# Kernel tuning notes

Hardware: AMD Instinct MI355X
Metric: run time of the kernel (lower is better)

Reference implementation:

```python
import math
import jax, jax.numpy as jnp
import numpy as np

LN_EPS = 1e-5


def _layernorm(x, g, b):
    m = jnp.mean(x, axis=-1, keepdims=True)
    v = jnp.var(x, axis=-1, keepdims=True)
    return (x - m) / jnp.sqrt(v + LN_EPS) * g + b


def setup_inputs() -> dict:
    key = jax.random.key(0)
    ks = jax.random.split(key, 14)
    B, C, H, W = 8, 96, 224, 224
    dim, hidden = 96, int(96 * 4.0)

    def lin(k, i, o):
        return jax.random.normal(k, (i, o), jnp.float32) * 0.02

    return {
        "x": jax.random.normal(ks[0], (B, C, H, W), jnp.float32),
        "entropy_map": jax.random.uniform(ks[1], (B, 1, H, W), jnp.float32),
        "beta": jnp.float32(1.0),
        "wq": lin(ks[2], dim, dim), "bq": jnp.zeros((dim,), jnp.float32),
        "wk": lin(ks[3], dim, dim), "bk": jnp.zeros((dim,), jnp.float32),
        "wv": lin(ks[4], dim, dim), "bv": jnp.zeros((dim,), jnp.float32),
        "wo": lin(ks[5], dim, dim), "bo": jnp.zeros((dim,), jnp.float32),
        "ln1_g": jnp.ones((dim,), jnp.float32), "ln1_b": jnp.zeros((dim,), jnp.float32),
        "ln2_g": jnp.ones((dim,), jnp.float32), "ln2_b": jnp.zeros((dim,), jnp.float32),
        "w_fc1": lin(ks[6], dim, hidden), "b_fc1": jnp.zeros((hidden,), jnp.float32),
        "w_fc2": lin(ks[7], hidden, dim), "b_fc2": jnp.zeros((dim,), jnp.float32),
    }


def reference(x, entropy_map, beta, wq, bq, wk, bk, wv, bv, wo, bo,
              ln1_g, ln1_b, ln2_g, ln2_b, w_fc1, b_fc1, w_fc2, b_fc2):
    B, C, H, W = x.shape
    ws = 7
    num_heads = 4
    hd = C // num_heads
    nHw, nWw = H // ws, W // ws
    N = ws * ws

    # (B,C,H,W) -> (B,H,W,C), norm1
    xt = jnp.transpose(x, (0, 2, 3, 1))
    xn = _layernorm(xt, ln1_g, ln1_b)

    # window partition -> (B*nW, N, C)
    xw = xn.reshape(B, nHw, ws, nWw, ws, C).transpose(0, 1, 3, 2, 4, 5).reshape(-1, N, C)
    ew = entropy_map.transpose(0, 2, 3, 1).reshape(B, nHw, ws, nWw, ws, 1)
    ew = ew.transpose(0, 1, 3, 2, 4, 5).reshape(-1, N, 1)  # (Bw, N, 1)

    Bw = xw.shape[0]
    q = (jnp.einsum('bnc,cd->bnd', xw, wq) + bq).reshape(Bw, N, num_heads, hd).transpose(0, 2, 1, 3)
    k = (jnp.einsum('bnc,cd->bnd', xw, wk) + bk).reshape(Bw, N, num_heads, hd).transpose(0, 2, 1, 3)
    v = (jnp.einsum('bnc,cd->bnd', xw, wv) + bv).reshape(Bw, N, num_heads, hd).transpose(0, 2, 1, 3)

    scores = jnp.einsum('bhqd,bhkd->bhqk', q, k) / math.sqrt(hd)
    attn = jax.nn.softmax(scores, axis=-1)

    # entropy gating: per-query factor (Bw,1,N,1), then renormalize over keys
    gating = jnp.exp(-beta * ew)[:, None, :, :]
    attn = attn * gating
    attn = attn / (jnp.sum(attn, axis=-1, keepdims=True) + 1e-9)

    out = jnp.einsum('bhqk,bhkd->bhqd', attn, v).transpose(0, 2, 1, 3).reshape(Bw, N, C)
    out = jnp.einsum('bnc,cd->bnd', out, wo) + bo

    # window merge -> (B,H,W,C)
    out = out.reshape(B, nHw, nWw, ws, ws, C).transpose(0, 1, 3, 2, 4, 5).reshape(B, H, W, C)

    x_res = xt + out  # (B,H,W,C)

    # MLP branch
    xn2 = _layernorm(x_res, ln2_g, ln2_b)
    h = jax.nn.gelu(jnp.einsum('bhwc,cd->bhwd', xn2, w_fc1) + b_fc1, approximate=False)
    mlp_out = jnp.einsum('bhwd,dc->bhwc', h, w_fc2) + b_fc2

    x_out = x_res + mlp_out
    return jnp.transpose(x_out, (0, 3, 1, 2))  # (B,C,H,W)
```

## Files before the change

### kernel.cpp

```cpp
#include <hip/hip_runtime.h>
#include <hip/hip_bf16.h>
#include <math.h>

typedef __attribute__((ext_vector_type(8))) short short8;
typedef __attribute__((ext_vector_type(4))) float f32x4;
typedef __attribute__((ext_vector_type(4))) unsigned int uint4v;

struct __align__(8) U2 { unsigned int x, y; };

#define DEVI static __device__ __forceinline__

DEVI unsigned pk1(float f){ unsigned u = __float_as_uint(f); return (u + 0x7fffu + ((u>>16)&1u)) >> 16; }
DEVI unsigned pk2(float a, float b){
  __hip_bfloat162 h = __float22bfloat162_rn(float2{a, b});
  union { __hip_bfloat162 h; unsigned u; } c; c.h = h; return c.u;
}
DEVI float bfu(unsigned hs){ return __uint_as_float((hs & 0xffffu) << 16); }

DEVI short8 lds8(const unsigned short* p){
  union { short8 v; U2 u[2]; } f;
  f.u[0] = *(const U2*)p;
  f.u[1] = *(const U2*)(p + 4);
  return f.v;
}
DEVI short8 mk8(unsigned a, unsigned b, unsigned c, unsigned d){
  union { short8 v; unsigned u[4]; } f; f.u[0]=a; f.u[1]=b; f.u[2]=c; f.u[3]=d; return f.v;
}
DEVI short8 zero8(){ return mk8(0,0,0,0); }
DEVI short8 gfrag(const unsigned short* p){ union { short8 v; uint4v u; } f; f.u = *(const uint4v*)p; return f.v; }
DEVI f32x4 MFMA(short8 a, short8 b, f32x4 c){ return __builtin_amdgcn_mfma_f32_16x16x32_bf16(a, b, c, 0, 0, 0); }
DEVI void st2(unsigned short* p, unsigned lo, unsigned hi){ U2 t; t.x=lo; t.y=hi; *(U2*)p = t; }

DEVI float fastrcp(float x){ float r; asm("v_rcp_f32 %0, %1" : "=v"(r) : "v"(x)); return r; }
DEVI float gelu_f(float v){
  float z2 = fmaf(v*v*v, -0.07135481627f, -1.5957691216f*v);
  return v * fastrcp(1.f + __expf(z2));
}

__global__ __launch_bounds__(256) void prep_kernel(
    const float* __restrict__ wq, const float* __restrict__ wk,
    const float* __restrict__ wv, const float* __restrict__ wo,
    const float* __restrict__ w1, const float* __restrict__ w2,
    unsigned short* __restrict__ wfr)
{
  int i = blockIdx.x * 256 + threadIdx.x;
  if (i >= 110592) return;
  int j = i & 7, lane = (i >> 3) & 63, fr = i >> 9;
  int ln = lane & 15, lg = lane >> 4;
  float v;
  if (fr < 18)      { int s = fr;       int mt = s/3,  kb = s%3;  v = wq[(32*kb + 8*lg + j)*96  + 16*mt + ln] * 0.20412414523193150818f; }
  else if (fr < 36) { int s = fr - 18;  int mt = s/3,  kb = s%3;  v = wk[(32*kb + 8*lg + j)*96  + 16*mt + ln]; }
  else if (fr < 54) { int s = fr - 36;  int mt = s/3,  kb = s%3;  v = wv[(32*kb + 8*lg + j)*96  + 16*mt + ln]; }
  else if (fr < 72) { int s = fr - 54;  int mt = s/3,  kb = s%3;  v = wo[(32*kb + 8*lg + j)*96  + 16*mt + ln]; }
  else if (fr < 144){ int s = fr - 72;  int mt = s/3,  kb = s%3;  v = w1[(32*kb + 8*lg + j)*384 + 16*mt + ln]; }
  else              { int s = fr - 144; int mt = s/12, kb = s%12; v = w2[(32*kb + 8*lg + j)*96  + 16*mt + ln]; }
  wfr[i] = (unsigned short)pk1(v);
}

__global__ __launch_bounds__(256, 4) void attn_kernel(
    const float* __restrict__ x, const float* __restrict__ emap,
    const float* __restrict__ beta_p,
    const float* __restrict__ bq, const float* __restrict__ bk,
    const float* __restrict__ bv, const float* __restrict__ bo,
    const float* __restrict__ g1, const float* __restrict__ b1,
    const unsigned short* __restrict__ wfr,
    unsigned short* __restrict__ xres)
{
  __shared__ __align__(16) char smem[39744];
  unsigned short* XN = (unsigned short*)(smem);
  unsigned short* VT = (unsigned short*)(smem);
  unsigned short* QS = (unsigned short*)(smem + 14144);
  unsigned short* KS = (unsigned short*)(smem + 26944);

  const int tid = threadIdx.x;
  const int lane = tid & 63;
  const int w = tid >> 6, lg = lane >> 4, ln = lane & 15;

  int bid = blockIdx.x;
  int bw  = ((bid & 7) << 10) | (bid >> 3);
  const int b  = bw >> 10;
  const int rr = bw & 1023;
  const int h0 = (rr >> 5) * 7;
  const int w0 = (rr & 31) * 7;

  const int t = 16*w + ln;

  float xv[24];
  float ewv = 0.f;
  {
    if (t < 49){
      size_t pixloc = (size_t)(h0 + t/7)*224 + w0 + t%7;
      const float* xp = x + (size_t)(b*96 + 4*lg)*50176 + pixloc;
#pragma unroll
      for (int mt = 0; mt < 6; ++mt)
#pragma unroll
        for (int r = 0; r < 4; ++r) xv[mt*4+r] = xp[(size_t)(16*mt + r)*50176];
      ewv = emap[(size_t)b*50176 + pixloc];
    } else {
#pragma unroll
      for (int i = 0; i < 24; ++i) xv[i] = 0.f;
    }
    float s = 0.f, s2 = 0.f;
#pragma unroll
    for (int i = 0; i < 24; ++i){ s += xv[i]; s2 += xv[i]*xv[i]; }
    s  += __shfl_xor(s, 16);  s  += __shfl_xor(s, 32);
    s2 += __shfl_xor(s2, 16); s2 += __shfl_xor(s2, 32);
    float m = s * (1.f/96.f);
    float var = s2 * (1.f/96.f) - m*m;
    float rstd = rsqrtf(var + 1e-5f);
    unsigned short* row = XN + t*100;
    if (t < 49){
#pragma unroll
      for (int mt = 0; mt < 6; ++mt){
        int c0 = 16*mt + 4*lg;
        st2(row + c0,
            pk2((xv[4*mt+0]-m)*rstd*g1[c0+0]+b1[c0+0], (xv[4*mt+1]-m)*rstd*g1[c0+1]+b1[c0+1]),
            pk2((xv[4*mt+2]-m)*rstd*g1[c0+2]+b1[c0+2], (xv[4*mt+3]-m)*rstd*g1[c0+3]+b1[c0+3]));
      }
    } else {
#pragma unroll
      for (int mt = 0; mt < 6; ++mt) st2(row + 16*mt + 4*lg, 0u, 0u);
    }
  }

  short8 bx0 = lds8(XN + t*100 + 0  + 8*lg);
  short8 bx1 = lds8(XN + t*100 + 32 + 8*lg);
  short8 bx2 = lds8(XN + t*100 + 64 + 8*lg);
  __syncthreads();

  {
#pragma unroll
    for (int mt = 0; mt < 6; ++mt){
      int d0 = 16*mt + 4*lg;
      f32x4 aq, ak;
#pragma unroll
      for (int r = 0; r < 4; ++r){ aq[r] = bq[d0+r]*0.20412414523193150818f; ak[r] = bk[d0+r]; }
      aq = MFMA(gfrag(wfr +        (mt*3+0)*512 + lane*8), bx0, aq);
      aq = MFMA(gfrag(wfr +        (mt*3+1)*512 + lane*8), bx1, aq);
      aq = MFMA(gfrag(wfr +        (mt*3+2)*512 + lane*8), bx2, aq);
      ak = MFMA(gfrag(wfr + 9216 + (mt*3+0)*512 + lane*8), bx0, ak);
      ak = MFMA(gfrag(wfr + 9216 + (mt*3+1)*512 + lane*8), bx1, ak);
      ak = MFMA(gfrag(wfr + 9216 + (mt*3+2)*512 + lane*8), bx2, ak);
      st2(QS + t*100 + d0, pk2(aq[0],aq[1]), pk2(aq[2],aq[3]));
      st2(KS + t*100 + d0, pk2(ak[0],ak[1]), pk2(ak[2],ak[3]));
    }
#pragma unroll
    for (int mt = 0; mt < 6; ++mt){
      int d0 = 16*mt + 4*lg;
      f32x4 av;
#pragma unroll
      for (int r = 0; r < 4; ++r) av[r] = bv[d0+r];
      av = MFMA(gfrag(wfr + 18432 + (mt*3+0)*512 + lane*8), bx0, av);
      av = MFMA(gfrag(wfr + 18432 + (mt*3+1)*512 + lane*8), bx1, av);
      av = MFMA(gfrag(wfr + 18432 + (mt*3+2)*512 + lane*8), bx2, av);
#pragma unroll
      for (int r = 0; r < 4; ++r) VT[(d0+r)*68 + t] = (unsigned short)pk1(av[r]);
    }
  }
  __syncthreads();

  const float beta = beta_p[0];
  const float gq   = __expf(-beta * ewv);
  const float gfac = gq / (gq + 1e-9f);
  const int  psrcA = ((lg & 1) << 5) + ln;
  const int  psrcB = psrcA + 16;
  const bool phi   = (lg >= 2);

  f32x4 mz;  mz[0]=0.f; mz[1]=0.f; mz[2]=0.f; mz[3]=0.f;
  f32x4 m3;
#pragma unroll
  for (int r = 0; r < 4; ++r) m3[r] = (4*lg + r >= 1) ? -50.f : 0.f;

#pragma unroll
  for (int h = 0; h < 4; ++h){
    short8 bqf = (lg < 3) ? lds8(QS + t*100 + 24*h + 8*lg) : zero8();
    f32x4 sva[4];
#pragma unroll
    for (int mt = 0; mt < 4; ++mt){
      short8 af = (lg < 3) ? lds8(KS + (16*mt+ln)*100 + 24*h + 8*lg) : zero8();
      sva[mt] = MFMA(af, bqf, (mt == 3) ? m3 : mz);
    }
    float vv[16]; float ssum = 0.f;
#pragma unroll
    for (int i = 0; i < 16; ++i){ float e = __expf(sva[i>>2][i&3]); vv[i] = e; ssum += e; }
    ssum += __shfl_xor(ssum, 16);
    ssum += __shfl_xor(ssum, 32);
    float inv = gfac * fastrcp(ssum);

    unsigned pu[4][2];
#pragma unroll
    for (int mt = 0; mt < 4; ++mt){
      pu[mt][0] = pk2(vv[4*mt+0], vv[4*mt+1]);
      pu[mt][1] = pk2(vv[4*mt+2], vv[4*mt+3]);
    }
    unsigned a00=__shfl(pu[0][0],psrcA), a01=__shfl(pu[0][1],psrcA);
    unsigned a10=__shfl(pu[1][0],psrcA), a11=__shfl(pu[1][1],psrcA);
    unsigned b00=__shfl(pu[0][0],psrcB), b01=__shfl(pu[0][1],psrcB);
    unsigned b10=__shfl(pu[1][0],psrcB), b11=__shfl(pu[1][1],psrcB);
    short8 pf0 = mk8(phi?a10:a00, phi?a11:a01, phi?b10:b00, phi?b11:b01);
    unsigned c00=__shfl(pu[2][0],psrcA), c01=__shfl(pu[2][1],psrcA);
    unsigned c10=__shfl(pu[3][0],psrcA), c11=__shfl(pu[3][1],psrcA);
    unsigned d00=__shfl(pu[2][0],psrcB), d01=__shfl(pu[2][1],psrcB);
    unsigned d10=__shfl(pu[3][0],psrcB), d11=__shfl(pu[3][1],psrcB);
    short8 pf1 = mk8(phi?c10:c00, phi?c11:c01, phi?d10:d00, phi?d11:d01);

#pragma unroll
    for (int mt = 0; mt < 2; ++mt){
      f32x4 pv; pv[0]=0.f; pv[1]=0.f; pv[2]=0.f; pv[3]=0.f;
      pv = MFMA(lds8(VT + (24*h+16*mt+ln)*68 + 0  + 8*lg), pf0, pv);
      pv = MFMA(lds8(VT + (24*h+16*mt+ln)*68 + 32 + 8*lg), pf1, pv);
      if (!(mt == 1 && lg >= 2))
        st2(QS + t*100 + 24*h + 16*mt + 4*lg,
            pk2(pv[0]*inv, pv[1]*inv), pk2(pv[2]*inv, pv[3]*inv));
    }
  }

  {
    f32x4 po[6];
#pragma unroll
    for (int mt = 0; mt < 6; ++mt){
      int c0 = 16*mt + 4*lg;
#pragma unroll
      for (int r = 0; r < 4; ++r) po[mt][r] = bo[c0+r];
    }
#pragma unroll
    for (int kb = 0; kb < 3; ++kb){
      short8 bf_ = lds8(QS + t*100 + 32*kb + 8*lg);
#pragma unroll
      for (int mt = 0; mt < 6; ++mt)
        po[mt] = MFMA(gfrag(wfr + 27648 + (mt*3+kb)*512 + lane*8), bf_, po[mt]);
    }
    if (t < 49){
      size_t pixloc = (size_t)(h0 + t/7)*224 + w0 + t%7;
      unsigned short* xo = xres + ((size_t)b*50176 + pixloc)*96;
#pragma unroll
      for (int mt = 0; mt < 6; ++mt){
        int c0 = 16*mt + 4*lg;
        st2(xo + c0,
            pk2(po[mt][0] + xv[4*mt+0], po[mt][1] + xv[4*mt+1]),
            pk2(po[mt][2] + xv[4*mt+2], po[mt][3] + xv[4*mt+3]));
      }
    }
  }
}

__global__ __launch_bounds__(256, 3) void mlp_kernel(
    const unsigned short* __restrict__ xres,
    const float* __restrict__ g2, const float* __restrict__ b2,
    const float* __restrict__ bf1, const float* __restrict__ bf2,
    const unsigned short* __restrict__ wfr,
    float* __restrict__ out)
{
  __shared__ __align__(16) unsigned short XH[4][6400];
  const int tid = threadIdx.x, lane = tid & 63, w = tid >> 6;
  const int lg = lane >> 4, ln = lane & 15;
  unsigned short* XN2 = &XH[w][0];
  unsigned short* HS  = &XH[w][3200];

  const int tile = blockIdx.x*4 + w;
  const size_t p0 = (size_t)tile * 32;
  const int bimg = (int)(p0 / 50176);
  const size_t pixin = p0 - (size_t)bimg*50176;

#pragma unroll
  for (int s = 0; s < 2; ++s){
    const unsigned* xp = (const unsigned*)(xres + (p0 + 16*s + (size_t)ln)*96 + 24*lg);
    float xv[24];
#pragma unroll
    for (int i = 0; i < 12; ++i){
      unsigned u = xp[i];
      xv[2*i] = bfu(u); xv[2*i+1] = bfu(u >> 16);
    }
    float sm = 0.f, s2 = 0.f;
#pragma unroll
    for (int i = 0; i < 24; ++i){ sm += xv[i]; s2 += xv[i]*xv[i]; }
    sm += __shfl_xor(sm, 16);  sm += __shfl_xor(sm, 32);
    s2 += __shfl_xor(s2, 16);  s2 += __shfl_xor(s2, 32);
    float m = sm * (1.f/96.f);
    float var = s2 * (1.f/96.f) - m*m;
    float rstd = rsqrtf(var + 1e-5f);
    unsigned* w32 = (unsigned*)(XN2 + (16*s + ln)*100 + 24*lg);
#pragma unroll
    for (int i = 0; i < 12; ++i){
      int c = 24*lg + 2*i;
      w32[i] = pk2((xv[2*i]   - m)*rstd*g2[c]   + b2[c],
                   (xv[2*i+1] - m)*rstd*g2[c+1] + b2[c+1]);
    }
  }

  f32x4 oaccA[6], oaccB[6];
#pragma unroll
  for (int mt = 0; mt < 6; ++mt){
    int c0 = 16*mt + 4*lg;
#pragma unroll
    for (int r = 0; r < 4; ++r){ oaccA[mt][r] = bf2[c0+r]; oaccB[mt][r] = bf2[c0+r]; }
  }

  short8 bxA0 = lds8(XN2 + ln*100 + 0  + 8*lg);
  short8 bxA1 = lds8(XN2 + ln*100 + 32 + 8*lg);
  short8 bxA2 = lds8(XN2 + ln*100 + 64 + 8*lg);
  short8 bxB0 = lds8(XN2 + (16+ln)*100 + 0  + 8*lg);
  short8 bxB1 = lds8(XN2 + (16+ln)*100 + 32 + 8*lg);
  short8 bxB2 = lds8(XN2 + (16+ln)*100 + 64 + 8*lg);

#pragma unroll
  for (int p = 0; p < 4; ++p){
#pragma unroll
    for (int mt = 0; mt < 6; ++mt){
      int hg = p*96 + 16*mt + 4*lg;
      f32x4 hA, hB;
#pragma unroll
      for (int r = 0; r < 4; ++r){ hA[r] = bf1[hg+r]; hB[r] = bf1[hg+r]; }
      short8 a0 = gfrag(wfr + 36864 + ((p*6+mt)*3+0)*512 + lane*8);
      short8 a1 = gfrag(wfr + 36864 + ((p*6+mt)*3+1)*512 + lane*8);
      short8 a2 = gfrag(wfr + 36864 + ((p*6+mt)*3+2)*512 + lane*8);
      hA = MFMA(a0, bxA0, hA); hB = MFMA(a0, bxB0, hB);
      hA = MFMA(a1, bxA1, hA); hB = MFMA(a1, bxB1, hB);
      hA = MFMA(a2, bxA2, hA); hB = MFMA(a2, bxB2, hB);
      st2(HS + ln*100 + 16*mt + 4*lg,
          pk2(gelu_f(hA[0]), gelu_f(hA[1])), pk2(gelu_f(hA[2]), gelu_f(hA[3])));
      st2(HS + (16+ln)*100 + 16*mt + 4*lg,
          pk2(gelu_f(hB[0]), gelu_f(hB[1])), pk2(gelu_f(hB[2]), gelu_f(hB[3])));
    }
#pragma unroll
    for (int kb = 0; kb < 3; ++kb){
      short8 bhA = lds8(HS + ln*100      + 32*kb + 8*lg);
      short8 bhB = lds8(HS + (16+ln)*100 + 32*kb + 8*lg);
#pragma unroll
      for (int mt = 0; mt < 6; ++mt){
        short8 af = gfrag(wfr + 73728 + (mt*12 + p*3 + kb)*512 + lane*8);
        oaccA[mt] = MFMA(af, bhA, oaccA[mt]);
        oaccB[mt] = MFMA(af, bhB, oaccB[mt]);
      }
    }
  }

  {
    const unsigned short* xrA = xres + (p0 + (size_t)ln)*96;
    const unsigned short* xrB = xrA + 16*96;
    float* obA = out + (size_t)bimg*96*50176 + pixin + ln;
    float* obB = obA + 16;
#pragma unroll
    for (int mt = 0; mt < 6; ++mt){
      int c0 = 16*mt + 4*lg;
      U2 rA = *(const U2*)(xrA + c0);
      U2 rB = *(const U2*)(xrB + c0);
      obA[(size_t)(c0+0)*50176] = oaccA[mt][0] + bfu(rA.x);
      obA[(size_t)(c0+1)*50176] = oaccA[mt][1] + bfu(rA.x >> 16);
      obA[(size_t)(c0+2)*50176] = oaccA[mt][2] + bfu(rA.y);
      obA[(size_t)(c0+3)*50176] = oaccA[mt][3] + bfu(rA.y >> 16);
      obB[(size_t)(c0+0)*50176] = oaccB[mt][0] + bfu(rB.x);
      obB[(size_t)(c0+1)*50176] = oaccB[mt][1] + bfu(rB.x >> 16);
      obB[(size_t)(c0+2)*50176] = oaccB[mt][2] + bfu(rB.y);
      obB[(size_t)(c0+3)*50176] = oaccB[mt][3] + bfu(rB.y >> 16);
    }
  }
}

extern "C" void kernel_launch(void* const* d_in, const int* in_sizes, int n_in,
                              void* d_out, int out_size, void* d_ws, size_t ws_size,
                              hipStream_t stream) {
  const float* x    = (const float*)d_in[0];
  const float* emap = (const float*)d_in[1];
  const float* beta = (const float*)d_in[2];
  const float* wq   = (const float*)d_in[3];
  const float* bq   = (const float*)d_in[4];
  const float* wk   = (const float*)d_in[5];
  const float* bk   = (const float*)d_in[6];
  const float* wv   = (const float*)d_in[7];
  const float* bv   = (const float*)d_in[8];
  const float* wo   = (const float*)d_in[9];
  const float* bo   = (const float*)d_in[10];
  const float* g1   = (const float*)d_in[11];
  const float* b1   = (const float*)d_in[12];
  const float* g2   = (const float*)d_in[13];
  const float* b2   = (const float*)d_in[14];
  const float* w1   = (const float*)d_in[15];
  const float* bf1  = (const float*)d_in[16];
  const float* w2   = (const float*)d_in[17];
  const float* bf2  = (const float*)d_in[18];

  float* out = (float*)d_out;
  unsigned short* wfr  = (unsigned short*)d_ws;
  unsigned short* xres = (unsigned short*)((char*)d_ws + 262144);

  prep_kernel<<<dim3(432), dim3(256), 0, stream>>>(wq, wk, wv, wo, w1, w2, wfr);
  attn_kernel<<<dim3(8192), dim3(256), 0, stream>>>(
      x, emap, beta, bq, bk, bv, bo, g1, b1, wfr, xres);
  mlp_kernel<<<dim3(3136), dim3(256), 0, stream>>>(
      xres, g2, b2, bf1, bf2, wfr, out);
}
```

Baseline: 408.4 us.

## Give V its own LDS region, compute V^T via swapped MFMA, pair heads

The V projection now gets its own shared-memory region instead of aliasing the normalized input. It is computed with swapped MFMA operands, so each wave writes V-transpose fragments with packed stores instead of scattered 16-bit stores. The attention loop handles two heads per iteration to raise instruction-level parallelism, and attention output is written into the freed input buffer. Shared memory grows and the occupancy hint drops from 4 to 3 blocks per CU, which risks less latency hiding.

New measurement: 349.7 us (median of 2 runs). 1.17x faster.

```diff
diff --git a/kernel.cpp b/kernel.cpp
--- a/kernel.cpp
+++ b/kernel.cpp
@@ -57,7 +57,7 @@
   wfr[i] = (unsigned short)pk1(v);
 }
 
-__global__ __launch_bounds__(256, 4) void attn_kernel(
+__global__ __launch_bounds__(256, 3) void attn_kernel(
     const float* __restrict__ x, const float* __restrict__ emap,
     const float* __restrict__ beta_p,
     const float* __restrict__ bq, const float* __restrict__ bk,
@@ -66,11 +66,11 @@
     const unsigned short* __restrict__ wfr,
     unsigned short* __restrict__ xres)
 {
-  __shared__ __align__(16) char smem[39744];
+  __shared__ __align__(16) char smem[52544];
   unsigned short* XN = (unsigned short*)(smem);
-  unsigned short* VT = (unsigned short*)(smem);
-  unsigned short* QS = (unsigned short*)(smem + 14144);
-  unsigned short* KS = (unsigned short*)(smem + 26944);
+  unsigned short* QS = (unsigned short*)(smem + 12800);
+  unsigned short* KS = (unsigned short*)(smem + 25600);
+  unsigned short* VT = (unsigned short*)(smem + 38400);
 
   const int tid = threadIdx.x;
   const int lane = tid & 63;
@@ -80,8 +80,8 @@
   int bw  = ((bid & 7) << 10) | (bid >> 3);
   const int b  = bw >> 10;
   const int rr = bw & 1023;
-  const int h0 = (rr >> 5) * 7;
-  const int w0 = (rr & 31) * 7;
+  const int h0w = (rr >> 5) * 7;
+  const int w0w = (rr & 31) * 7;
 
   const int t = 16*w + ln;
 
@@ -89,7 +89,7 @@
   float ewv = 0.f;
   {
     if (t < 49){
-      size_t pixloc = (size_t)(h0 + t/7)*224 + w0 + t%7;
+      size_t pixloc = (size_t)(h0w + t/7)*224 + w0w + t%7;
       const float* xp = x + (size_t)(b*96 + 4*lg)*50176 + pixloc;
 #pragma unroll
       for (int mt = 0; mt < 6; ++mt)
@@ -122,13 +122,12 @@
       for (int mt = 0; mt < 6; ++mt) st2(row + 16*mt + 4*lg, 0u, 0u);
     }
   }
-
-  short8 bx0 = lds8(XN + t*100 + 0  + 8*lg);
-  short8 bx1 = lds8(XN + t*100 + 32 + 8*lg);
-  short8 bx2 = lds8(XN + t*100 + 64 + 8*lg);
   __syncthreads();
 
   {
+    short8 bx0 = lds8(XN + t*100 + 0  + 8*lg);
+    short8 bx1 = lds8(XN + t*100 + 32 + 8*lg);
+    short8 bx2 = lds8(XN + t*100 + 64 + 8*lg);
 #pragma unroll
     for (int mt = 0; mt < 6; ++mt){
       int d0 = 16*mt + 4*lg;
@@ -145,16 +144,16 @@
       st2(KS + t*100 + d0, pk2(ak[0],ak[1]), pk2(ak[2],ak[3]));
     }
 #pragma unroll
-    for (int mt = 0; mt < 6; ++mt){
-      int d0 = 16*mt + 4*lg;
-      f32x4 av;
-#pragma unroll
-      for (int r = 0; r < 4; ++r) av[r] = bv[d0+r];
-      av = MFMA(gfrag(wfr + 18432 + (mt*3+0)*512 + lane*8), bx0, av);
-      av = MFMA(gfrag(wfr + 18432 + (mt*3+1)*512 + lane*8), bx1, av);
-      av = MFMA(gfrag(wfr + 18432 + (mt*3+2)*512 + lane*8), bx2, av);
-#pragma unroll
-      for (int r = 0; r < 4; ++r) VT[(d0+r)*68 + t] = (unsigned short)pk1(av[r]);
+    for (int f = 0; f < 6; ++f){
+      int fl = f*4 + w;
+      int mt = fl / 6, nt = fl % 6;
+      float bvv = bv[16*nt + ln];
+      f32x4 av; av[0]=bvv; av[1]=bvv; av[2]=bvv; av[3]=bvv;
+#pragma unroll
+      for (int kb = 0; kb < 3; ++kb)
+        av = MFMA(lds8(XN + (16*mt+ln)*100 + 32*kb + 8*lg),
+                  gfrag(wfr + 18432 + (nt*3+kb)*512 + lane*8), av);
+      st2(VT + (16*nt+ln)*68 + 16*mt + 4*lg, pk2(av[0],av[1]), pk2(av[2],av[3]));
     }
   }
   __syncthreads();
@@ -172,46 +171,77 @@
   for (int r = 0; r < 4; ++r) m3[r] = (4*lg + r >= 1) ? -50.f : 0.f;
 
 #pragma unroll
-  for (int h = 0; h < 4; ++h){
-    short8 bqf = (lg < 3) ? lds8(QS + t*100 + 24*h + 8*lg) : zero8();
-    f32x4 sva[4];
+  for (int hp = 0; hp < 2; ++hp){
+    const int h0 = 2*hp, h1 = 2*hp + 1;
+
+    short8 bqf0 = (lg < 3) ? lds8(QS + t*100 + 24*h0 + 8*lg) : zero8();
+    short8 bqf1 = (lg < 3) ? lds8(QS + t*100 + 24*h1 + 8*lg) : zero8();
+    f32x4 sv0[4], sv1[4];
 #pragma unroll
     for (int mt = 0; mt < 4; ++mt){
-      short8 af = (lg < 3) ? lds8(KS + (16*mt+ln)*100 + 24*h + 8*lg) : zero8();
-      sva[mt] = MFMA(af, bqf, (mt == 3) ? m3 : mz);
-    }
-    float vv[16]; float ssum = 0.f;
-#pragma unroll
-    for (int i = 0; i < 16; ++i){ float e = __expf(sva[i>>2][i&3]); vv[i] = e; ssum += e; }
-    ssum += __shfl_xor(ssum, 16);
-    ssum += __shfl_xor(ssum, 32);
-    float inv = gfac * fastrcp(ssum);
-
-    unsigned pu[4][2];
+      short8 af0 = (lg < 3) ? lds8(KS + (16*mt+ln)*100 + 24*h0 + 8*lg) : zero8();
+      short8 af1 = (lg < 3) ? lds8(KS + (16*mt+ln)*100 + 24*h1 + 8*lg) : zero8();
+      f32x4 ci = (mt == 3) ? m3 : mz;
+      sv0[mt] = MFMA(af0, bqf0, ci);
+      sv1[mt] = MFMA(af1, bqf1, ci);
+    }
+
+    float vv0[16], vv1[16];
+    float ss0 = 0.f, ss1 = 0.f;
+#pragma unroll
+    for (int i = 0; i < 16; ++i){
+      float e0 = __expf(sv0[i>>2][i&3]); vv0[i] = e0; ss0 += e0;
+      float e1 = __expf(sv1[i>>2][i&3]); vv1[i] = e1; ss1 += e1;
+    }
+    ss0 += __shfl_xor(ss0, 16);  ss1 += __shfl_xor(ss1, 16);
+    ss0 += __shfl_xor(ss0, 32);  ss1 += __shfl_xor(ss1, 32);
+    float inv0 = gfac * fastrcp(ss0);
+    float inv1 = gfac * fastrcp(ss1);
+
+    unsigned pu0[4][2], pu1[4][2];
 #pragma unroll
     for (int mt = 0; mt < 4; ++mt){
-      pu[mt][0] = pk2(vv[4*mt+0], vv[4*mt+1]);
-      pu[mt][1] = pk2(vv[4*mt+2], vv[4*mt+3]);
-    }
-    unsigned a00=__shfl(pu[0][0],psrcA), a01=__shfl(pu[0][1],psrcA);
-    unsigned a10=__shfl(pu[1][0],psrcA), a11=__shfl(pu[1][1],psrcA);
-    unsigned b00=__shfl(pu[0][0],psrcB), b01=__shfl(pu[0][1],psrcB);
-    unsigned b10=__shfl(pu[1][0],psrcB), b11=__shfl(pu[1][1],psrcB);
-    short8 pf0 = mk8(phi?a10:a00, phi?a11:a01, phi?b10:b00, phi?b11:b01);
-    unsigned c00=__shfl(pu[2][0],psrcA), c01=__shfl(pu[2][1],psrcA);
-    unsigned c10=__shfl(pu[3][0],psrcA), c11=__shfl(pu[3][1],psrcA);
-    unsigned d00=__shfl(pu[2][0],psrcB), d01=__shfl(pu[2][1],psrcB);
-    unsigned d10=__shfl(pu[3][0],psrcB), d11=__shfl(pu[3][1],psrcB);
-    short8 pf1 = mk8(phi?c10:c00, phi?c11:c01, phi?d10:d00, phi?d11:d01);
+      pu0[mt][0] = pk2(vv0[4*mt+0], vv0[4*mt+1]);
+      pu0[mt][1] = pk2(vv0[4*mt+2], vv0[4*mt+3]);
+      pu1[mt][0] = pk2(vv1[4*mt+0], vv1[4*mt+1]);
+      pu1[mt][1] = pk2(vv1[4*mt+2], vv1[4*mt+3]);
+    }
+
+    unsigned a00=__shfl(pu0[0][0],psrcA), a01=__shfl(pu0[0][1],psrcA);
+    unsigned e00=__shfl(pu1[0][0],psrcA), e01=__shfl(pu1[0][1],psrcA);
+    unsigned a10=__shfl(pu0[1][0],psrcA), a11=__shfl(pu0[1][1],psrcA);
+    unsigned e10=__shfl(pu1[1][0],psrcA), e11=__shfl(pu1[1][1],psrcA);
+    unsigned b00=__shfl(pu0[0][0],psrcB), b01=__shfl(pu0[0][1],psrcB);
+    unsigned f00=__shfl(pu1[0][0],psrcB), f01=__shfl(pu1[0][1],psrcB);
+    unsigned b10=__shfl(pu0[1][0],psrcB), b11=__shfl(pu0[1][1],psrcB);
+    unsigned f10=__shfl(pu1[1][0],psrcB), f11=__shfl(pu1[1][1],psrcB);
+    short8 pf00 = mk8(phi?a10:a00, phi?a11:a01, phi?b10:b00, phi?b11:b01);
+    short8 pf10 = mk8(phi?e10:e00, phi?e11:e01, phi?f10:f00, phi?f11:f01);
+    unsigned c00=__shfl(pu0[2][0],psrcA), c01=__shfl(pu0[2][1],psrcA);
+    unsigned g00=__shfl(pu1[2][0],psrcA), g01=__shfl(pu1[2][1],psrcA);
+    unsigned c10=__shfl(pu0[3][0],psrcA), c11=__shfl(pu0[3][1],psrcA);
+    unsigned g10=__shfl(pu1[3][0],psrcA), g11=__shfl(pu1[3][1],psrcA);
+    unsigned d00=__shfl(pu0[2][0],psrcB), d01=__shfl(pu0[2][1],psrcB);
+    unsigned k00=__shfl(pu1[2][0],psrcB), k01=__shfl(pu1[2][1],psrcB);
+    unsigned d10=__shfl(pu0[3][0],psrcB), d11=__shfl(pu0[3][1],psrcB);
+    unsigned k10=__shfl(pu1[3][0],psrcB), k11=__shfl(pu1[3][1],psrcB);
+    short8 pf01 = mk8(phi?c10:c00, phi?c11:c01, phi?d10:d00, phi?d11:d01);
+    short8 pf11 = mk8(phi?g10:g00, phi?g11:g01, phi?k10:k00, phi?k11:k01);
 
 #pragma unroll
     for (int mt = 0; mt < 2; ++mt){
-      f32x4 pv; pv[0]=0.f; pv[1]=0.f; pv[2]=0.f; pv[3]=0.f;
-      pv = MFMA(lds8(VT + (24*h+16*mt+ln)*68 + 0  + 8*lg), pf0, pv);
-      pv = MFMA(lds8(VT + (24*h+16*mt+ln)*68 + 32 + 8*lg), pf1, pv);
-      if (!(mt == 1 && lg >= 2))
-        st2(QS + t*100 + 24*h + 16*mt + 4*lg,
-            pk2(pv[0]*inv, pv[1]*inv), pk2(pv[2]*inv, pv[3]*inv));
+      f32x4 pv0; pv0[0]=0.f; pv0[1]=0.f; pv0[2]=0.f; pv0[3]=0.f;
+      f32x4 pv1; pv1[0]=0.f; pv1[1]=0.f; pv1[2]=0.f; pv1[3]=0.f;
+      pv0 = MFMA(lds8(VT + (24*h0+16*mt+ln)*68 + 0  + 8*lg), pf00, pv0);
+      pv1 = MFMA(lds8(VT + (24*h1+16*mt+ln)*68 + 0  + 8*lg), pf10, pv1);
+      pv0 = MFMA(lds8(VT + (24*h0+16*mt+ln)*68 + 32 + 8*lg), pf01, pv0);
+      pv1 = MFMA(lds8(VT + (24*h1+16*mt+ln)*68 + 32 + 8*lg), pf11, pv1);
+      if (!(mt == 1 && lg >= 2)){
+        st2(XN + t*100 + 24*h0 + 16*mt + 4*lg,
+            pk2(pv0[0]*inv0, pv0[1]*inv0), pk2(pv0[2]*inv0, pv0[3]*inv0));
+        st2(XN + t*100 + 24*h1 + 16*mt + 4*lg,
+            pk2(pv1[0]*inv1, pv1[1]*inv1), pk2(pv1[2]*inv1, pv1[3]*inv1));
+      }
     }
   }
 
@@ -225,13 +255,13 @@
     }
 #pragma unroll
     for (int kb = 0; kb < 3; ++kb){
-      short8 bf_ = lds8(QS + t*100 + 32*kb + 8*lg);
+      short8 bf_ = lds8(XN + t*100 + 32*kb + 8*lg);
 #pragma unroll
       for (int mt = 0; mt < 6; ++mt)
         po[mt] = MFMA(gfrag(wfr + 27648 + (mt*3+kb)*512 + lane*8), bf_, po[mt]);
     }
     if (t < 49){
-      size_t pixloc = (size_t)(h0 + t/7)*224 + w0 + t%7;
+      size_t pixloc = (size_t)(h0w + t/7)*224 + w0w + t%7;
       unsigned short* xo = xres + ((size_t)b*50176 + pixloc)*96;
 #pragma unroll
       for (int mt = 0; mt < 6; ++mt){
```
